# Performance work log

Measured on AMD Instinct MI355X. Metric: run time of the kernel, lower is better.

Reference implementation:

```python
import jax, jax.numpy as jnp
import numpy as np

EPS = 1e-5
N_GROUP = 1

def _linear(x, w, b):
    # w: [in, out], b: [out]
    return x @ w + b

def _group_norm_per_sample(x, weight, bias, n_group=N_GROUP, eps=EPS):
    # x: [B, C]; weight/bias: [B, C] (per-sample hypernet-generated affine).
    # F.group_norm on 2D input normalizes each sample over its channel groups.
    B, C = x.shape
    xr = x.reshape(B, n_group, C // n_group)
    m = jnp.mean(xr, axis=-1, keepdims=True)
    v = jnp.mean((xr - m) ** 2, axis=-1, keepdims=True)
    xn = ((xr - m) * jax.lax.rsqrt(v + eps)).reshape(B, C)
    return xn * weight + bias

def setup_inputs() -> dict:
    key = jax.random.key(0)
    ks = jax.random.split(key, 32)
    B, P, CIN, COUT = 32768, 8, 512, 256
    s = 0.05
    d = {}
    d['x_feature'] = jax.random.normal(ks[0], (B, CIN), dtype=jnp.float32)
    d['x_param'] = jax.random.normal(ks[1], (B, P), dtype=jnp.float32)
    # hypernet for norm1 weight/bias (P -> 32 -> 2048)
    d['hw1_1_w'] = jax.random.normal(ks[2], (P, 32)) * s;   d['hw1_1_b'] = jnp.zeros((32,))
    d['hw1_2_w'] = jax.random.normal(ks[3], (32, 2048)) * s; d['hw1_2_b'] = jnp.ones((2048,))
    d['hb1_1_w'] = jax.random.normal(ks[4], (P, 32)) * s;   d['hb1_1_b'] = jnp.zeros((32,))
    d['hb1_2_w'] = jax.random.normal(ks[5], (32, 2048)) * s; d['hb1_2_b'] = jnp.zeros((2048,))
    # hypernet for norm2 weight/bias (P -> 32 -> 1024)
    d['hw2_1_w'] = jax.random.normal(ks[6], (P, 32)) * s;   d['hw2_1_b'] = jnp.zeros((32,))
    d['hw2_2_w'] = jax.random.normal(ks[7], (32, 1024)) * s; d['hw2_2_b'] = jnp.ones((1024,))
    d['hb2_1_w'] = jax.random.normal(ks[8], (P, 32)) * s;   d['hb2_1_b'] = jnp.zeros((32,))
    d['hb2_2_w'] = jax.random.normal(ks[9], (32, 1024)) * s; d['hb2_2_b'] = jnp.zeros((1024,))
    # base net
    d['l1_w'] = jax.random.normal(ks[10], (CIN, 2048)) * s;  d['l1_b'] = jnp.zeros((2048,))
    d['l2_w'] = jax.random.normal(ks[11], (2048, 1024)) * s; d['l2_b'] = jnp.zeros((1024,))
    d['l3_w'] = jax.random.normal(ks[12], (1024, COUT)) * s; d['l3_b'] = jnp.zeros((COUT,))
    return d

def reference(x_feature, x_param,
              hw1_1_w, hw1_1_b, hw1_2_w, hw1_2_b,
              hb1_1_w, hb1_1_b, hb1_2_w, hb1_2_b,
              hw2_1_w, hw2_1_b, hw2_2_w, hw2_2_b,
              hb2_1_w, hb2_1_b, hb2_2_w, hb2_2_b,
              l1_w, l1_b, l2_w, l2_b, l3_w, l3_b):
    # hypernet: per-sample group-norm affine params
    p = x_param  # already n_level columns
    w1 = _linear(jax.nn.relu(_linear(p, hw1_1_w, hw1_1_b)), hw1_2_w, hw1_2_b)  # [B, 2048]
    b1 = _linear(jax.nn.relu(_linear(p, hb1_1_w, hb1_1_b)), hb1_2_w, hb1_2_b)  # [B, 2048]
    w2 = _linear(jax.nn.relu(_linear(p, hw2_1_w, hw2_1_b)), hw2_2_w, hw2_2_b)  # [B, 1024]
    b2 = _linear(jax.nn.relu(_linear(p, hb2_1_w, hb2_1_b)), hb2_2_w, hb2_2_b)  # [B, 1024]
    # base net with per-sample affine group norm (vectorized form of the torch
    # host-side grouping loop: samples with identical x_param share identical
    # generated affine params, and group_norm stats are per-sample anyway)
    x = _linear(x_feature, l1_w, l1_b)            # [B, 2048]
    x = jax.nn.relu(_group_norm_per_sample(x, w1, b1))
    x = _linear(x, l2_w, l2_b)                    # [B, 1024]
    x = jax.nn.relu(_group_norm_per_sample(x, w2, b2))
    x = _linear(x, l3_w, l3_b)                    # [B, 256]
    return jax.nn.log_softmax(x, axis=1)
```

## Files before the change

kernel.cpp:

```cpp
#include <hip/hip_runtime.h>

typedef unsigned short u16;
typedef float f32x4 __attribute__((ext_vector_type(4)));
typedef __bf16 bf16x8 __attribute__((ext_vector_type(8)));
typedef u16 u16x4 __attribute__((ext_vector_type(4)));
typedef u16 u16x8 __attribute__((ext_vector_type(8)));

__device__ __forceinline__ float bf2f(u16 u) {
    unsigned int x = ((unsigned int)u) << 16;
    return __builtin_bit_cast(float, x);
}
__device__ __forceinline__ u16 f2bf(float f) {
    unsigned int x = __builtin_bit_cast(unsigned int, f);
    x += 0x7fffu + ((x >> 16) & 1u);
    return (u16)(x >> 16);
}

#define GLD16(gp, lp)                                                          \
    __builtin_amdgcn_global_load_lds(                                          \
        (const __attribute__((address_space(1))) void*)(gp),                   \
        (__attribute__((address_space(3))) void*)(lp), 16, 0, 0)

__global__ void f32_to_bf16_k(const float* __restrict__ in, u16* __restrict__ out, long n4) {
    long i = (long)blockIdx.x * 256 + threadIdx.x;
    if (i >= n4) return;
    f32x4 v = *reinterpret_cast<const f32x4*>(in + i * 4);
    u16x4 o;
    o[0] = f2bf(v[0]); o[1] = f2bf(v[1]); o[2] = f2bf(v[2]); o[3] = f2bf(v[3]);
    *reinterpret_cast<u16x4*>(out + i * 4) = o;
}

__global__ void transpose_f32_bf16(const float* __restrict__ in, u16* __restrict__ out,
                                   int R, int C) {
    __shared__ float tile[32][33];
    const int bx = blockIdx.x * 32;
    const int by = blockIdx.y * 32;
    const int tx = threadIdx.x;
    const int ty0 = threadIdx.y;
    #pragma unroll
    for (int ty = ty0; ty < 32; ty += 8)
        tile[ty][tx] = in[(long)(by + ty) * C + bx + tx];
    __syncthreads();
    #pragma unroll
    for (int ty = ty0; ty < 32; ty += 8)
        out[(long)(bx + ty) * R + by + tx] = f2bf(tile[tx][ty]);
}

__global__ void hyper_h4(const float* __restrict__ P,
                         const float* __restrict__ Wa, const float* __restrict__ ba, u16* __restrict__ Ha,
                         const float* __restrict__ Wb, const float* __restrict__ bb_, u16* __restrict__ Hb,
                         const float* __restrict__ Wc, const float* __restrict__ bc, u16* __restrict__ Hc,
                         const float* __restrict__ Wd, const float* __restrict__ bd, u16* __restrict__ Hd,
                         int B_) {
    const int idx = blockIdx.x * 256 + threadIdx.x;
    if (idx >= B_ * 32) return;
    const int s = idx >> 5, c = idx & 31;
    float p[8];
    #pragma unroll
    for (int k = 0; k < 8; ++k) p[k] = P[s * 8 + k];
    auto one = [&](const float* W, const float* b, u16* H) {
        float a = b[c];
        #pragma unroll
        for (int k = 0; k < 8; ++k) a += p[k] * W[k * 32 + c];
        H[idx] = f2bf(fmaxf(a, 0.f));
    };
    one(Wa, ba, Ha); one(Wb, bb_, Hb); one(Wc, bc, Hc); one(Wd, bd, Hd);
}

template <int OUT_BF16, int STATS>
__global__ __launch_bounds__(512, 2) void gemm256(
    const u16* __restrict__ A, const u16* __restrict__ BT,
    const float* __restrict__ bias, u16* __restrict__ Cb, float* __restrict__ Cf,
    float* __restrict__ stats, int M, int N, int K, int mblocks) {
    __shared__ __align__(16) u16 lds[2][2][2][128 * 64];
    const int tid = threadIdx.x;
    const int lane = tid & 63;
    const int wave = tid >> 6;
    const int wr = wave & 1;
    const int wc = wave >> 1;

    const int nwg = gridDim.x;
    const int bid = blockIdx.x;
    const int swz = (bid & 7) * (nwg >> 3) + (bid >> 3);
    const int bx = swz % mblocks;
    const int by = swz / mblocks;
    const long row0 = (long)bx * 256;
    const long col0 = (long)by * 256;

    const int srow = tid >> 3;
    const int scb = ((tid & 7) * 16) ^ (((tid >> 5) & 1) << 5);
    const long sAoff = (row0 + srow) * (long)K + (scb >> 1);
    const long sBoff = (col0 + srow) * (long)K + (scb >> 1);

    auto STAGE = [&](int buf, int ab, int half, int kt) {
        const u16* g = (ab ? BT : A) + (ab ? sBoff : sAoff) + (long)half * 128 * K + (long)kt * 64;
        u16* d = &lds[buf][ab][half][tid * 8];
        GLD16(g, d);
        GLD16(g + 64 * (long)K, d + 4096);
    };

    const int ln15 = lane & 15, ln16 = lane >> 4;
    const int swz_b = ((ln15 >> 2) & 1) << 5;
    const int cbe0 = ((ln16 * 16) ^ swz_b) >> 1;
    const int arow = (wr * 64 + ln15) * 64;
    const int brow = (wc * 32 + ln15) * 64;

    f32x4 acc[8][4] = {};

#define PHASE(BUF, AH, BH, SAB, SH, KT)                                          \
    {                                                                            \
        asm volatile("s_waitcnt vmcnt(4)" ::: "memory");                         \
        __builtin_amdgcn_sched_barrier(0);                                       \
        __builtin_amdgcn_s_barrier();                                            \
        __builtin_amdgcn_sched_barrier(0);                                       \
        STAGE((BUF) ^ 1, SAB, SH, KT);                                           \
        bf16x8 aF[4][2], bF[2][2];                                               \
        const u16* ap = &lds[BUF][0][AH][0];                                     \
        const u16* bp = &lds[BUF][1][BH][0];                                     \
        _Pragma("unroll") for (int ml = 0; ml < 4; ++ml)                         \
            _Pragma("unroll") for (int kk = 0; kk < 2; ++kk)                     \
                aF[ml][kk] = *(const bf16x8*)(ap + arow + ml * 1024 + cbe0 + kk * 32); \
        _Pragma("unroll") for (int nl = 0; nl < 2; ++nl)                         \
            _Pragma("unroll") for (int kk = 0; kk < 2; ++kk)                     \
                bF[nl][kk] = *(const bf16x8*)(bp + brow + nl * 1024 + cbe0 + kk * 32); \
        __builtin_amdgcn_s_setprio(1);                                           \
        _Pragma("unroll") for (int ml = 0; ml < 4; ++ml)                         \
            _Pragma("unroll") for (int nl = 0; nl < 2; ++nl)                     \
                _Pragma("unroll") for (int kk = 0; kk < 2; ++kk)                 \
                    acc[(AH) * 4 + ml][(BH) * 2 + nl] =                          \
                        __builtin_amdgcn_mfma_f32_16x16x32_bf16(                 \
                            aF[ml][kk], bF[nl][kk], acc[(AH) * 4 + ml][(BH) * 2 + nl], 0, 0, 0); \
        __builtin_amdgcn_s_setprio(0);                                           \
    }

    STAGE(0, 0, 0, 0); STAGE(0, 1, 0, 0); STAGE(0, 0, 1, 0); STAGE(0, 1, 1, 0);

    const int nt = K >> 6;
    for (int it = 0; it < (nt >> 1); ++it) {
        const int t0 = it * 2;
        const int ka = t0 + 1;
        const int kb = (t0 + 2 < nt) ? t0 + 2 : nt - 1;
        PHASE(0, 0, 0, 0, 0, ka)
        PHASE(0, 1, 0, 1, 0, ka)
        PHASE(0, 1, 1, 0, 1, ka)
        PHASE(0, 0, 1, 1, 1, ka)
        PHASE(1, 0, 0, 0, 0, kb)
        PHASE(1, 1, 0, 1, 0, kb)
        PHASE(1, 1, 1, 0, 1, kb)
        PHASE(1, 0, 1, 1, 1, kb)
    }
#undef PHASE
    asm volatile("s_waitcnt vmcnt(0)" ::: "memory");

    float bv[4];
    #pragma unroll
    for (int n = 0; n < 4; ++n)
        bv[n] = bias[col0 + wc * 32 + (n & 1) * 16 + (n >> 1) * 128 + ln15];

    #pragma unroll
    for (int m = 0; m < 8; ++m) {
        const long rowb = row0 + wr * 64 + (m & 3) * 16 + (m >> 2) * 128 + ln16 * 4;
        #pragma unroll
        for (int n = 0; n < 4; ++n) {
            const long col = col0 + wc * 32 + (n & 1) * 16 + (n >> 1) * 128 + ln15;
            #pragma unroll
            for (int r = 0; r < 4; ++r) {
                const float v = acc[m][n][r] + bv[n];
                if (OUT_BF16) Cb[(rowb + r) * (long)N + col] = f2bf(v);
                else          Cf[(rowb + r) * (long)N + col] = v;
            }
        }
        if (STATS) {
            #pragma unroll
            for (int r = 0; r < 4; ++r) {
                float s = 0.f, ss = 0.f;
                #pragma unroll
                for (int n = 0; n < 4; ++n) {
                    const float v = acc[m][n][r] + bv[n];
                    s += v; ss += v * v;
                }
                #pragma unroll
                for (int d = 1; d < 16; d <<= 1) { s += __shfl_xor(s, d); ss += __shfl_xor(ss, d); }
                if (ln15 == 0) {
                    float* sp = stats + (((long)by * 4 + wc) * M + rowb + r) * 2;
                    sp[0] = s; sp[1] = ss;
                }
            }
        }
    }
}

template <int C, int NPART>
__global__ __launch_bounds__(256, 2) void gn_affine(
    u16* __restrict__ Y, const float* __restrict__ stats, int Btot,
    const u16* __restrict__ Hw, const u16* __restrict__ Hb,
    const u16* __restrict__ WwT, const u16* __restrict__ WbT,
    const float* __restrict__ bw, const float* __restrict__ bb) {
    const int tid = threadIdx.x;
    const int lane = tid & 63;
    const int wave = tid >> 6;
    const long r0 = (long)blockIdx.x * 32;
    __shared__ float mean_l[32], rs_l[32];
    __shared__ __align__(16) float wt[32][132];
    __shared__ __align__(16) float btl[32][132];

    const int row = tid >> 3, sub = tid & 7;

    {
        float s = 0.f, ss = 0.f;
        for (int p_ = sub; p_ < NPART; p_ += 8) {
            const float* sp = stats + ((long)p_ * Btot + (r0 + row)) * 2;
            s += sp[0]; ss += sp[1];
        }
        s  += __shfl_xor(s, 1);  s  += __shfl_xor(s, 2);  s  += __shfl_xor(s, 4);
        ss += __shfl_xor(ss, 1); ss += __shfl_xor(ss, 2); ss += __shfl_xor(ss, 4);
        if (sub == 0) {
            float m = s / (float)C;
            float var = fmaxf(ss / (float)C - m * m, 0.f);
            mean_l[row] = m;
            rs_l[row] = rsqrtf(var + 1e-5f);
        }
    }
    __syncthreads();

    const int mm = wave & 1;
    const int npair = wave >> 1;
    const bf16x8 ha = *reinterpret_cast<const bf16x8*>(
        Hw + (r0 + mm * 16 + (lane & 15)) * 32 + (lane >> 4) * 8);
    const bf16x8 hbf = *reinterpret_cast<const bf16x8*>(
        Hb + (r0 + mm * 16 + (lane & 15)) * 32 + (lane >> 4) * 8);

    for (int c0 = 0; c0 < C; c0 += 128) {
        #pragma unroll
        for (int j = 0; j < 4; ++j) {
            const int n = npair * 4 + j;
            const int cl = c0 + n * 16 + (lane & 15);
            const bf16x8 wv = *reinterpret_cast<const bf16x8*>(WwT + (long)cl * 32 + (lane >> 4) * 8);
            const bf16x8 bv = *reinterpret_cast<const bf16x8*>(WbT + (long)cl * 32 + (lane >> 4) * 8);
            f32x4 z = {0.f, 0.f, 0.f, 0.f};
            f32x4 wa = __builtin_amdgcn_mfma_f32_16x16x32_bf16(ha, wv, z, 0, 0, 0);
            f32x4 ba = __builtin_amdgcn_mfma_f32_16x16x32_bf16(hbf, bv, z, 0, 0, 0);
            const float bwv = bw[cl], bbv = bb[cl];
            const int ncol = n * 16 + (lane & 15);
            #pragma unroll
            for (int r = 0; r < 4; ++r) {
                const int rl = mm * 16 + (lane >> 4) * 4 + r;
                wt[rl][ncol]  = wa[r] + bwv;
                btl[rl][ncol] = ba[r] + bbv;
            }
        }
        __syncthreads();
        {
            const long base = (r0 + row) * (long)C + c0 + sub * 16;
            u16x8 v0 = *reinterpret_cast<const u16x8*>(Y + base);
            u16x8 v1 = *reinterpret_cast<const u16x8*>(Y + base + 8);
            const float mu = mean_l[row], rs = rs_l[row];
            u16x8 o0, o1;
            #pragma unroll
            for (int j = 0; j < 8; ++j) {
                float f = (bf2f(v0[j]) - mu) * rs;
                f = f * wt[row][sub * 16 + j] + btl[row][sub * 16 + j];
                o0[j] = f2bf(fmaxf(f, 0.f));
                float g = (bf2f(v1[j]) - mu) * rs;
                g = g * wt[row][sub * 16 + 8 + j] + btl[row][sub * 16 + 8 + j];
                o1[j] = f2bf(fmaxf(g, 0.f));
            }
            *reinterpret_cast<u16x8*>(Y + base) = o0;
            *reinterpret_cast<u16x8*>(Y + base + 8) = o1;
        }
        __syncthreads();
    }
}

template <int OUT_BF16>
__global__ __launch_bounds__(256, 2) void gemm_bt(
    const u16* __restrict__ A, const u16* __restrict__ BT,
    const float* __restrict__ bias, u16* __restrict__ Cb, float* __restrict__ Cf,
    int M, int N, int K) {
    __shared__ __align__(16) u16 As[128 * 64];
    __shared__ __align__(16) u16 Bs[128 * 64];
    const int tid = threadIdx.x;
    const int lane = tid & 63;
    const int wave = tid >> 6;
    const int wr = wave >> 1, wc = wave & 1;
    const long row0 = (long)blockIdx.x * 128;
    const long col0 = (long)blockIdx.y * 128;

    const int srow = tid >> 3;
    const int scol = (tid & 7) * 8;
    const u16* Ag = A + (row0 + srow) * (long)K + scol;
    const u16* Bg = BT + (col0 + srow) * (long)K + scol;
    u16* AsW = As + (size_t)(wave * 64) * 8;
    u16* BsW = Bs + (size_t)(wave * 64) * 8;

    f32x4 acc[4][4] = {};

    for (int k0 = 0; k0 < K; k0 += 64) {
        #pragma unroll
        for (int i = 0; i < 4; ++i) {
            GLD16(Ag + (long)i * 32 * K + k0, AsW + i * 256 * 8);
            GLD16(Bg + (long)i * 32 * K + k0, BsW + i * 256 * 8);
        }
        __syncthreads();
        #pragma unroll
        for (int kk = 0; kk < 2; ++kk) {
            bf16x8 af[4], bfr[4];
            #pragma unroll
            for (int m = 0; m < 4; ++m)
                af[m] = *reinterpret_cast<const bf16x8*>(
                    As + (wr * 64 + m * 16 + (lane & 15)) * 64 + kk * 32 + (lane >> 4) * 8);
            #pragma unroll
            for (int n = 0; n < 4; ++n)
                bfr[n] = *reinterpret_cast<const bf16x8*>(
                    Bs + (wc * 64 + n * 16 + (lane & 15)) * 64 + kk * 32 + (lane >> 4) * 8);
            #pragma unroll
            for (int m = 0; m < 4; ++m)
                #pragma unroll
                for (int n = 0; n < 4; ++n)
                    acc[m][n] = __builtin_amdgcn_mfma_f32_16x16x32_bf16(af[m], bfr[n],
                                                                        acc[m][n], 0, 0, 0);
        }
        __syncthreads();
    }

    #pragma unroll
    for (int n = 0; n < 4; ++n) {
        const long col = col0 + wc * 64 + n * 16 + (lane & 15);
        const float bvv = bias[col];
        #pragma unroll
        for (int m = 0; m < 4; ++m) {
            const long rowb = row0 + wr * 64 + m * 16 + ((lane >> 4) * 4);
            #pragma unroll
            for (int r = 0; r < 4; ++r) {
                const float v = acc[m][n][r] + bvv;
                if (OUT_BF16) Cb[(rowb + r) * (long)N + col] = f2bf(v);
                else          Cf[(rowb + r) * (long)N + col] = v;
            }
        }
    }
}

__global__ __launch_bounds__(256) void logsoftmax256(const float* __restrict__ X,
                                                     float* __restrict__ O) {
    const int wave = threadIdx.x >> 6, lane = threadIdx.x & 63;
    const long row = (long)blockIdx.x * 4 + wave;
    const float* x = X + row * 256 + lane * 4;
    f32x4 v = *reinterpret_cast<const f32x4*>(x);
    float mx = fmaxf(fmaxf(v[0], v[1]), fmaxf(v[2], v[3]));
    #pragma unroll
    for (int d = 1; d < 64; d <<= 1) mx = fmaxf(mx, __shfl_xor(mx, d));
    float s = 0.f;
    #pragma unroll
    for (int j = 0; j < 4; ++j) s += __expf(v[j] - mx);
    #pragma unroll
    for (int d = 1; d < 64; d <<= 1) s += __shfl_xor(s, d);
    const float lse = mx + logf(s);
    f32x4 o;
    #pragma unroll
    for (int j = 0; j < 4; ++j) o[j] = v[j] - lse;
    *reinterpret_cast<f32x4*>(O + row * 256 + lane * 4) = o;
}

extern "C" void kernel_launch(void* const* d_in, const int* in_sizes, int n_in,
                              void* d_out, int out_size, void* d_ws, size_t ws_size,
                              hipStream_t stream) {
    const float* x_feature = (const float*)d_in[0];
    const float* x_param   = (const float*)d_in[1];
    const float* hw1_1_w = (const float*)d_in[2];
    const float* hw1_1_b = (const float*)d_in[3];
    const float* hw1_2_w = (const float*)d_in[4];
    const float* hw1_2_b = (const float*)d_in[5];
    const float* hb1_1_w = (const float*)d_in[6];
    const float* hb1_1_b = (const float*)d_in[7];
    const float* hb1_2_w = (const float*)d_in[8];
    const float* hb1_2_b = (const float*)d_in[9];
    const float* hw2_1_w = (const float*)d_in[10];
    const float* hw2_1_b = (const float*)d_in[11];
    const float* hw2_2_w = (const float*)d_in[12];
    const float* hw2_2_b = (const float*)d_in[13];
    const float* hb2_1_w = (const float*)d_in[14];
    const float* hb2_1_b = (const float*)d_in[15];
    const float* hb2_2_w = (const float*)d_in[16];
    const float* hb2_2_b = (const float*)d_in[17];
    const float* l1_w = (const float*)d_in[18];
    const float* l1_b = (const float*)d_in[19];
    const float* l2_w = (const float*)d_in[20];
    const float* l2_b = (const float*)d_in[21];
    const float* l3_w = (const float*)d_in[22];
    const float* l3_b = (const float*)d_in[23];

    const int B = in_sizes[0] / 512;
    constexpr int CIN = 512, C1 = 2048, C2 = 1024, COUT = 256;

    char* p = (char*)d_ws;
    auto carve = [&](size_t bytes) {
        char* q = p;
        p += (bytes + 255) & ~(size_t)255;
        return q;
    };
    u16* xb    = (u16*)carve((size_t)B * CIN * 2);
    u16* y1    = (u16*)carve((size_t)B * C1 * 2);
    u16* y2    = (u16*)carve((size_t)B * C2 * 2);
    u16* w1T   = (u16*)carve((size_t)C1 * CIN * 2);
    u16* w2T   = (u16*)carve((size_t)C2 * C1 * 2);
    u16* w3T   = (u16*)carve((size_t)COUT * C2 * 2);
    u16* hw12T = (u16*)carve((size_t)C1 * 32 * 2);
    u16* hb12T = (u16*)carve((size_t)C1 * 32 * 2);
    u16* hw22T = (u16*)carve((size_t)C2 * 32 * 2);
    u16* hb22T = (u16*)carve((size_t)C2 * 32 * 2);
    u16* Hw1   = (u16*)carve((size_t)B * 32 * 2);
    u16* Hb1   = (u16*)carve((size_t)B * 32 * 2);
    u16* Hw2   = (u16*)carve((size_t)B * 32 * 2);
    u16* Hb2   = (u16*)carve((size_t)B * 32 * 2);
    float* stat1 = (float*)carve((size_t)(C1 / 256) * 4 * B * 2 * 4);
    float* stat2 = (float*)carve((size_t)(C2 / 256) * 4 * B * 2 * 4);
    float* logits = (float*)y1;

    f32_to_bf16_k<<<(B * CIN / 4 + 255) / 256, 256, 0, stream>>>(x_feature, xb, (long)B * CIN / 4);
    dim3 tb(32, 8);
    transpose_f32_bf16<<<dim3(C1 / 32, CIN / 32), tb, 0, stream>>>(l1_w, w1T, CIN, C1);
    transpose_f32_bf16<<<dim3(C2 / 32, C1 / 32), tb, 0, stream>>>(l2_w, w2T, C1, C2);
    transpose_f32_bf16<<<dim3(COUT / 32, C2 / 32), tb, 0, stream>>>(l3_w, w3T, C2, COUT);
    transpose_f32_bf16<<<dim3(C1 / 32, 1), tb, 0, stream>>>(hw1_2_w, hw12T, 32, C1);
    transpose_f32_bf16<<<dim3(C1 / 32, 1), tb, 0, stream>>>(hb1_2_w, hb12T, 32, C1);
    transpose_f32_bf16<<<dim3(C2 / 32, 1), tb, 0, stream>>>(hw2_2_w, hw22T, 32, C2);
    transpose_f32_bf16<<<dim3(C2 / 32, 1), tb, 0, stream>>>(hb2_2_w, hb22T, 32, C2);
    hyper_h4<<<B * 32 / 256, 256, 0, stream>>>(x_param,
        hw1_1_w, hw1_1_b, Hw1, hb1_1_w, hb1_1_b, Hb1,
        hw2_1_w, hw2_1_b, Hw2, hb2_1_w, hb2_1_b, Hb2, B);

    gemm256<1, 1><<<(B / 256) * (C1 / 256), 512, 0, stream>>>(
        xb, w1T, l1_b, y1, nullptr, stat1, B, C1, CIN, B / 256);
    gn_affine<C1, (C1 / 256) * 4><<<B / 32, 256, 0, stream>>>(
        y1, stat1, B, Hw1, Hb1, hw12T, hb12T, hw1_2_b, hb1_2_b);
    gemm256<1, 1><<<(B / 256) * (C2 / 256), 512, 0, stream>>>(
        y1, w2T, l2_b, y2, nullptr, stat2, B, C2, C1, B / 256);
    gn_affine<C2, (C2 / 256) * 4><<<B / 32, 256, 0, stream>>>(
        y2, stat2, B, Hw2, Hb2, hw22T, hb22T, hw2_2_b, hb2_2_b);
    gemm_bt<0><<<dim3(B / 128, COUT / 128), 256, 0, stream>>>(
        y2, w3T, l3_b, nullptr, logits, B, COUT, C2);
    logsoftmax256<<<B / 4, 256, 0, stream>>>(logits, (float*)d_out);
}
```

Before: 599.6 us.

## Fuse final GEMM with log-softmax and switch LDS swizzle to XOR-8 pattern

Replaces the separate final GEMM and log-softmax kernels with a gemm256 variant that computes row max, sum-exp and log-sum-exp in its epilogue through LDS reductions across the four column waves. This drops the fp32 logits round-trip through global memory and one launch. It also changes the LDS swizzle for all gemm256 instances from a 1-bit XOR to a full 3-bit XOR over 16-byte chunks, to cut bank conflicts on fragment reads. The final GEMM now runs only 128 blocks of 512 threads, which may underfill the GPU.

```diff
diff --git a/kernel.cpp b/kernel.cpp
--- a/kernel.cpp
+++ b/kernel.cpp
@@ -67,7 +67,7 @@
     one(Wa, ba, Ha); one(Wb, bb_, Hb); one(Wc, bc, Hc); one(Wd, bd, Hd);
 }
 
-template <int OUT_BF16, int STATS>
+template <int OUT_BF16, int STATS, int LSM>
 __global__ __launch_bounds__(512, 2) void gemm256(
     const u16* __restrict__ A, const u16* __restrict__ BT,
     const float* __restrict__ bias, u16* __restrict__ Cb, float* __restrict__ Cf,
@@ -88,9 +88,9 @@
     const long col0 = (long)by * 256;
 
     const int srow = tid >> 3;
-    const int scb = ((tid & 7) * 16) ^ (((tid >> 5) & 1) << 5);
-    const long sAoff = (row0 + srow) * (long)K + (scb >> 1);
-    const long sBoff = (col0 + srow) * (long)K + (scb >> 1);
+    const int selem = (((tid & 7) ^ ((tid >> 3) & 7)) << 3);
+    const long sAoff = (row0 + srow) * (long)K + selem;
+    const long sBoff = (col0 + srow) * (long)K + selem;
 
     auto STAGE = [&](int buf, int ab, int half, int kt) {
         const u16* g = (ab ? BT : A) + (ab ? sBoff : sAoff) + (long)half * 128 * K + (long)kt * 64;
@@ -100,8 +100,8 @@
     };
 
     const int ln15 = lane & 15, ln16 = lane >> 4;
-    const int swz_b = ((ln15 >> 2) & 1) << 5;
-    const int cbe0 = ((ln16 * 16) ^ swz_b) >> 1;
+    const int c0e = ((ln16)     ^ (ln15 & 7)) << 3;
+    const int c1e = ((ln16 + 4) ^ (ln15 & 7)) << 3;
     const int arow = (wr * 64 + ln15) * 64;
     const int brow = (wc * 32 + ln15) * 64;
 
@@ -117,12 +117,14 @@
         bf16x8 aF[4][2], bF[2][2];                                               \
         const u16* ap = &lds[BUF][0][AH][0];                                     \
         const u16* bp = &lds[BUF][1][BH][0];                                     \
-        _Pragma("unroll") for (int ml = 0; ml < 4; ++ml)                         \
-            _Pragma("unroll") for (int kk = 0; kk < 2; ++kk)                     \
-                aF[ml][kk] = *(const bf16x8*)(ap + arow + ml * 1024 + cbe0 + kk * 32); \
-        _Pragma("unroll") for (int nl = 0; nl < 2; ++nl)                         \
-            _Pragma("unroll") for (int kk = 0; kk < 2; ++kk)                     \
-                bF[nl][kk] = *(const bf16x8*)(bp + brow + nl * 1024 + cbe0 + kk * 32); \
+        _Pragma("unroll") for (int ml = 0; ml < 4; ++ml) {                       \
+            aF[ml][0] = *(const bf16x8*)(ap + arow + ml * 1024 + c0e);           \
+            aF[ml][1] = *(const bf16x8*)(ap + arow + ml * 1024 + c1e);           \
+        }                                                                        \
+        _Pragma("unroll") for (int nl = 0; nl < 2; ++nl) {                       \
+            bF[nl][0] = *(const bf16x8*)(bp + brow + nl * 1024 + c0e);           \
+            bF[nl][1] = *(const bf16x8*)(bp + brow + nl * 1024 + c1e);           \
+        }                                                                        \
         __builtin_amdgcn_s_setprio(1);                                           \
         _Pragma("unroll") for (int ml = 0; ml < 4; ++ml)                         \
             _Pragma("unroll") for (int nl = 0; nl < 2; ++nl)                     \
@@ -157,6 +159,67 @@
     for (int n = 0; n < 4; ++n)
         bv[n] = bias[col0 + wc * 32 + (n & 1) * 16 + (n >> 1) * 128 + ln15];
 
+    if constexpr (LSM) {
+        __syncthreads();
+        float* red  = (float*)&lds[0][0][0][0];
+        float* red2 = red + 1024;
+        #pragma unroll
+        for (int m = 0; m < 8; ++m)
+            #pragma unroll
+            for (int n = 0; n < 4; ++n)
+                #pragma unroll
+                for (int r = 0; r < 4; ++r)
+                    acc[m][n][r] += bv[n];
+        #pragma unroll
+        for (int m = 0; m < 8; ++m) {
+            const int rb = wr * 64 + (m & 3) * 16 + (m >> 2) * 128 + ln16 * 4;
+            #pragma unroll
+            for (int r = 0; r < 4; ++r) {
+                float mx = fmaxf(fmaxf(acc[m][0][r], acc[m][1][r]),
+                                 fmaxf(acc[m][2][r], acc[m][3][r]));
+                #pragma unroll
+                for (int d = 1; d < 16; d <<= 1) mx = fmaxf(mx, __shfl_xor(mx, d));
+                if (ln15 == 0) red[wc * 256 + rb + r] = mx;
+            }
+        }
+        __syncthreads();
+        float gmv[8][4];
+        #pragma unroll
+        for (int m = 0; m < 8; ++m) {
+            const int rb = wr * 64 + (m & 3) * 16 + (m >> 2) * 128 + ln16 * 4;
+            #pragma unroll
+            for (int r = 0; r < 4; ++r) {
+                float gm = fmaxf(fmaxf(red[rb + r], red[256 + rb + r]),
+                                 fmaxf(red[512 + rb + r], red[768 + rb + r]));
+                float se = 0.f;
+                #pragma unroll
+                for (int n = 0; n < 4; ++n) se += __expf(acc[m][n][r] - gm);
+                #pragma unroll
+                for (int d = 1; d < 16; d <<= 1) se += __shfl_xor(se, d);
+                if (ln15 == 0) red2[wc * 256 + rb + r] = se;
+                gmv[m][r] = gm;
+            }
+        }
+        __syncthreads();
+        #pragma unroll
+        for (int m = 0; m < 8; ++m) {
+            const int rb = wr * 64 + (m & 3) * 16 + (m >> 2) * 128 + ln16 * 4;
+            const long rowb = row0 + rb;
+            #pragma unroll
+            for (int r = 0; r < 4; ++r) {
+                const float gs = red2[rb + r] + red2[256 + rb + r] +
+                                 red2[512 + rb + r] + red2[768 + rb + r];
+                const float l = gmv[m][r] + __logf(gs);
+                #pragma unroll
+                for (int n = 0; n < 4; ++n) {
+                    const long col = wc * 32 + (n & 1) * 16 + (n >> 1) * 128 + ln15;
+                    Cf[(rowb + r) * (long)N + col] = acc[m][n][r] - l;
+                }
+            }
+        }
+        return;
+    }
+
     #pragma unroll
     for (int m = 0; m < 8; ++m) {
         const long rowb = row0 + wr * 64 + (m & 3) * 16 + (m >> 2) * 128 + ln16 * 4;
@@ -270,95 +333,6 @@
         }
         __syncthreads();
     }
-}
-
-template <int OUT_BF16>
-__global__ __launch_bounds__(256, 2) void gemm_bt(
-    const u16* __restrict__ A, const u16* __restrict__ BT,
-    const float* __restrict__ bias, u16* __restrict__ Cb, float* __restrict__ Cf,
-    int M, int N, int K) {
-    __shared__ __align__(16) u16 As[128 * 64];
-    __shared__ __align__(16) u16 Bs[128 * 64];
-    const int tid = threadIdx.x;
-    const int lane = tid & 63;
-    const int wave = tid >> 6;
-    const int wr = wave >> 1, wc = wave & 1;
-    const long row0 = (long)blockIdx.x * 128;
-    const long col0 = (long)blockIdx.y * 128;
-
-    const int srow = tid >> 3;
-    const int scol = (tid & 7) * 8;
-    const u16* Ag = A + (row0 + srow) * (long)K + scol;
-    const u16* Bg = BT + (col0 + srow) * (long)K + scol;
-    u16* AsW = As + (size_t)(wave * 64) * 8;
-    u16* BsW = Bs + (size_t)(wave * 64) * 8;
-
-    f32x4 acc[4][4] = {};
-
-    for (int k0 = 0; k0 < K; k0 += 64) {
-        #pragma unroll
-        for (int i = 0; i < 4; ++i) {
-            GLD16(Ag + (long)i * 32 * K + k0, AsW + i * 256 * 8);
-            GLD16(Bg + (long)i * 32 * K + k0, BsW + i * 256 * 8);
-        }
-        __syncthreads();
-        #pragma unroll
-        for (int kk = 0; kk < 2; ++kk) {
-            bf16x8 af[4], bfr[4];
-            #pragma unroll
-            for (int m = 0; m < 4; ++m)
-                af[m] = *reinterpret_cast<const bf16x8*>(
-                    As + (wr * 64 + m * 16 + (lane & 15)) * 64 + kk * 32 + (lane >> 4) * 8);
-            #pragma unroll
-            for (int n = 0; n < 4; ++n)
-                bfr[n] = *reinterpret_cast<const bf16x8*>(
-                    Bs + (wc * 64 + n * 16 + (lane & 15)) * 64 + kk * 32 + (lane >> 4) * 8);
-            #pragma unroll
-            for (int m = 0; m < 4; ++m)
-                #pragma unroll
-                for (int n = 0; n < 4; ++n)
-                    acc[m][n] = __builtin_amdgcn_mfma_f32_16x16x32_bf16(af[m], bfr[n],
-                                                                        acc[m][n], 0, 0, 0);
-        }
-        __syncthreads();
-    }
-
-    #pragma unroll
-    for (int n = 0; n < 4; ++n) {
-        const long col = col0 + wc * 64 + n * 16 + (lane & 15);
-        const float bvv = bias[col];
-        #pragma unroll
-        for (int m = 0; m < 4; ++m) {
-            const long rowb = row0 + wr * 64 + m * 16 + ((lane >> 4) * 4);
-            #pragma unroll
-            for (int r = 0; r < 4; ++r) {
-                const float v = acc[m][n][r] + bvv;
-                if (OUT_BF16) Cb[(rowb + r) * (long)N + col] = f2bf(v);
-                else          Cf[(rowb + r) * (long)N + col] = v;
-            }
-        }
-    }
-}
-
-__global__ __launch_bounds__(256) void logsoftmax256(const float* __restrict__ X,
-                                                     float* __restrict__ O) {
-    const int wave = threadIdx.x >> 6, lane = threadIdx.x & 63;
-    const long row = (long)blockIdx.x * 4 + wave;
-    const float* x = X + row * 256 + lane * 4;
-    f32x4 v = *reinterpret_cast<const f32x4*>(x);
-    float mx = fmaxf(fmaxf(v[0], v[1]), fmaxf(v[2], v[3]));
-    #pragma unroll
-    for (int d = 1; d < 64; d <<= 1) mx = fmaxf(mx, __shfl_xor(mx, d));
-    float s = 0.f;
-    #pragma unroll
-    for (int j = 0; j < 4; ++j) s += __expf(v[j] - mx);
-    #pragma unroll
-    for (int d = 1; d < 64; d <<= 1) s += __shfl_xor(s, d);
-    const float lse = mx + logf(s);
-    f32x4 o;
-    #pragma unroll
-    for (int j = 0; j < 4; ++j) o[j] = v[j] - lse;
-    *reinterpret_cast<f32x4*>(O + row * 256 + lane * 4) = o;
 }
 
 extern "C" void kernel_launch(void* const* d_in, const int* in_sizes, int n_in,
@@ -414,7 +388,6 @@
     u16* Hb2   = (u16*)carve((size_t)B * 32 * 2);
     float* stat1 = (float*)carve((size_t)(C1 / 256) * 4 * B * 2 * 4);
     float* stat2 = (float*)carve((size_t)(C2 / 256) * 4 * B * 2 * 4);
-    float* logits = (float*)y1;
 
     f32_to_bf16_k<<<(B * CIN / 4 + 255) / 256, 256, 0, stream>>>(x_feature, xb, (long)B * CIN / 4);
     dim3 tb(32, 8);
@@ -429,15 +402,14 @@
         hw1_1_w, hw1_1_b, Hw1, hb1_1_w, hb1_1_b, Hb1,
         hw2_1_w, hw2_1_b, Hw2, hb2_1_w, hb2_1_b, Hb2, B);
 
-    gemm256<1, 1><<<(B / 256) * (C1 / 256), 512, 0, stream>>>(
+    gemm256<1, 1, 0><<<(B / 256) * (C1 / 256), 512, 0, stream>>>(
         xb, w1T, l1_b, y1, nullptr, stat1, B, C1, CIN, B / 256);
     gn_affine<C1, (C1 / 256) * 4><<<B / 32, 256, 0, stream>>>(
         y1, stat1, B, Hw1, Hb1, hw12T, hb12T, hw1_2_b, hb1_2_b);
-    gemm256<1, 1><<<(B / 256) * (C2 / 256), 512, 0, stream>>>(
+    gemm256<1, 1, 0><<<(B / 256) * (C2 / 256), 512, 0, stream>>>(
         y1, w2T, l2_b, y2, nullptr, stat2, B, C2, C1, B / 256);
     gn_affine<C2, (C2 / 256) * 4><<<B / 32, 256, 0, stream>>>(
         y2, stat2, B, Hw2, Hb2, hw22T, hb22T, hw2_2_b, hb2_2_b);
-    gemm_bt<0><<<dim3(B / 128, COUT / 128), 256, 0, stream>>>(
-        y2, w3T, l3_b, nullptr, logits, B, COUT, C2);
-    logsoftmax256<<<B / 4, 256, 0, stream>>>(logits, (float*)d_out);
-}
+    gemm256<0, 0, 1><<<(B / 256) * (COUT / 256), 512, 0, stream>>>(
+        y2, w3T, l3_b, nullptr, (float*)d_out, nullptr, B, COUT, C2, B / 256);
+}
```

After: 562.7 us. 1.07x faster.
